# Performance work log

Hardware: AMD Instinct MI355X
Metric: run time of the kernel (lower is better)

The kernel has to match this reference:

```python
import jax, jax.numpy as jnp
import numpy as np

B, L = 512, 8192          # batch, document length
N = 128                   # output_sentence_num
S = 256                   # output_sentence_len
DELIM = 5                 # delimiter token
PAD = 0                   # pad_word
CUT_HEAD = False
VOCAB = 100


def setup_inputs() -> dict:
    key = jax.random.key(0)
    x = jax.random.randint(key, (B, L), 0, VOCAB, dtype=jnp.int32)
    return {"x": x}


def reference(x):
    b, l = x.shape
    # right-padded row: original tokens + one trailing delimiter, shape [B, L+1]
    rpad = jnp.concatenate([x, jnp.full((b, 1), DELIM, x.dtype)], axis=1)
    # segment id of rpad position j = number of delimiters in x[:j]
    cum = jnp.cumsum((x == DELIM).astype(jnp.int32), axis=1)           # [B, L]
    seg = jnp.concatenate([jnp.zeros((b, 1), jnp.int32), cum], axis=1)  # [B, L+1]
    seg = jnp.minimum(seg, N - 1)  # segments >= N-1 merged into last chunk (tail merge)
    j = jnp.arange(l + 1, dtype=jnp.int32)
    bidx = jnp.arange(b)[:, None]
    # start index of each segment (min j with seg==k); unused segments stay at L+1
    starts = jnp.full((b, N), l + 1, jnp.int32)
    starts = starts.at[bidx, seg].min(jnp.broadcast_to(j, (b, l + 1)))
    pos = j[None, :] - jnp.take_along_axis(starts, seg, axis=1)  # offset within chunk
    # chunk sizes (number of rpad positions per segment)
    sizes = jnp.zeros((b, N), jnp.int32).at[bidx, seg].add(jnp.ones((b, l + 1), jnp.int32))
    size_here = jnp.take_along_axis(sizes, seg, axis=1)
    # size-1 chunks (lone delimiter == empty sentence) are filled with pad_word
    vals = jnp.where(size_here == 1, jnp.int32(PAD), rpad)
    if CUT_HEAD:
        p = pos - 1
        valid = (pos >= 1) & (pos <= S - 1)  # chunk[1:S], then padded to S
    else:
        p = pos
        valid = pos <= S - 1                 # chunk[:S]
    # scatter into [B, N, S]; invalid positions routed out-of-bounds and dropped
    k_idx = jnp.where(valid, seg, N)
    p_idx = jnp.where(valid, p, S)
    otp = jnp.full((b, N, S), PAD, x.dtype)
    otp = otp.at[bidx, k_idx, p_idx].set(vals, mode='drop')
    # lengths / mask (tf.count_nonzero semantics; pad_word == 0)
    len_sent = jnp.sum((otp != 0).astype(jnp.int32), axis=2)   # [B, N]
    len_doc = jnp.sum((len_sent != 0).astype(jnp.int32), axis=1)  # [B]
    mask = (jnp.arange(S)[None, None, :] < len_sent[..., None]).astype(jnp.float32)
    return otp, len_doc, mask
```

## Files before the change

### kernel.cpp

```cpp
#include <hip/hip_runtime.h>

#define B_ 512
#define L_ 8192
#define N_ 128
#define S_ 256
#define DELIM_ 5
#define T_ 1024
#define NW_ (T_ / 64)

__device__ __forceinline__ int sw_idx(int p) { return p ^ ((p >> 5) & 3); }

__global__ __launch_bounds__(T_, 8) void split_kernel(const int* __restrict__ x,
                                                      float* __restrict__ otp,
                                                      float* __restrict__ len_doc,
                                                      float* __restrict__ mask) {
    const int b = blockIdx.x;
    const int t = threadIdx.x;
    const int lane = t & 63;
    const int w = t >> 6;
    const int* __restrict__ row = x + (size_t)b * L_;

    __shared__ __align__(16) int s_row[L_ + 1];
    __shared__ int s_wsum[NW_];
    __shared__ int s_dpos[N_ - 1];
    __shared__ int s_start[N_];
    __shared__ int s_cl[N_];
    __shared__ int s_doc[NW_];

    const int4 r0 = ((const int4*)row)[t];
    const int4 r1 = ((const int4*)row)[t + T_];

    const int v = (t >> 3) & 3;
    int4 w0 = r0, w1 = r1;
    if (v == 1)      { w0 = make_int4(r0.y, r0.x, r0.w, r0.z); w1 = make_int4(r1.y, r1.x, r1.w, r1.z); }
    else if (v == 2) { w0 = make_int4(r0.z, r0.w, r0.x, r0.y); w1 = make_int4(r1.z, r1.w, r1.x, r1.y); }
    else if (v == 3) { w0 = make_int4(r0.w, r0.z, r0.y, r0.x); w1 = make_int4(r1.w, r1.z, r1.y, r1.x); }
    ((int4*)s_row)[t] = w0;
    ((int4*)s_row)[t + T_] = w1;
    if (t == 0) s_row[L_] = DELIM_;

    const int c0 = (r0.x == DELIM_) + (r0.y == DELIM_) + (r0.z == DELIM_) + (r0.w == DELIM_);
    const int c1 = (r1.x == DELIM_) + (r1.y == DELIM_) + (r1.z == DELIM_) + (r1.w == DELIM_);
    const int packed = c0 | (c1 << 16);

    int sv = packed;
#pragma unroll
    for (int d = 1; d < 64; d <<= 1) {
        int n = __shfl_up(sv, d, 64);
        if (lane >= d) sv += n;
    }
    if (lane == 63) s_wsum[w] = sv;
    __syncthreads();

    int woff = 0, tot = 0;
#pragma unroll
    for (int i = 0; i < NW_; ++i) {
        const int s = s_wsum[i];
        if (i < w) woff += s;
        tot += s;
    }
    const int pre = woff + sv - packed;
    const int c0tot = tot & 0xffff;
    const int m = c0tot + (tot >> 16);
    const int off0 = pre & 0xffff;
    const int off1 = c0tot + (pre >> 16);

    if (c0 > 0 && off0 < N_ - 1) {
        int o = off0;
        const int p = 4 * t;
        if (r0.x == DELIM_) { if (o < N_ - 1) s_dpos[o] = p;     ++o; }
        if (r0.y == DELIM_) { if (o < N_ - 1) s_dpos[o] = p + 1; ++o; }
        if (r0.z == DELIM_) { if (o < N_ - 1) s_dpos[o] = p + 2; ++o; }
        if (r0.w == DELIM_) { if (o < N_ - 1) s_dpos[o] = p + 3; ++o; }
    }
    if (c1 > 0 && off1 < N_ - 1) {
        int o = off1;
        const int p = 4 * T_ + 4 * t;
        if (r1.x == DELIM_) { if (o < N_ - 1) s_dpos[o] = p;     ++o; }
        if (r1.y == DELIM_) { if (o < N_ - 1) s_dpos[o] = p + 1; ++o; }
        if (r1.z == DELIM_) { if (o < N_ - 1) s_dpos[o] = p + 2; ++o; }
        if (r1.w == DELIM_) { if (o < N_ - 1) s_dpos[o] = p + 3; ++o; }
    }
    __syncthreads();

    if (t < N_) {
        const int k = t;
        const int mc = (m < N_ - 1) ? m : (N_ - 1);
        int start = 0, cl = 0;
        if (k <= mc) {
            start = (k == 0) ? 0 : (s_dpos[k - 1] + 1);
            const int end = (k < mc) ? s_dpos[k] : L_;
            const int size = end - start + 1;
            cl = (size <= 1) ? 0 : (size < S_ ? size : S_);
        }
        s_start[k] = start;
        s_cl[k] = cl;
    }
    __syncthreads();

    float* __restrict__ otp_b = otp + (size_t)b * N_ * S_;
    float* __restrict__ msk_b = mask + (size_t)b * N_ * S_;
    int doccnt = 0;
    const int e0 = lane << 2;
#pragma unroll
    for (int i = 0; i < (N_ / NW_); ++i) {
        const int k = i * NW_ + w;
        const int start = s_start[k];
        const int cl = s_cl[k];
        float4 tf = make_float4(0.f, 0.f, 0.f, 0.f);
        float4 mk = make_float4(0.f, 0.f, 0.f, 0.f);
        int len = 0;
        if (cl > 0) {
            int t0 = 0, t1 = 0, t2 = 0, t3 = 0;
            if (e0 + 0 < cl) t0 = s_row[sw_idx(start + e0 + 0)];
            if (e0 + 1 < cl) t1 = s_row[sw_idx(start + e0 + 1)];
            if (e0 + 2 < cl) t2 = s_row[sw_idx(start + e0 + 2)];
            if (e0 + 3 < cl) t3 = s_row[sw_idx(start + e0 + 3)];
            len += __popcll(__ballot(t0 != 0));
            len += __popcll(__ballot(t1 != 0));
            len += __popcll(__ballot(t2 != 0));
            len += __popcll(__ballot(t3 != 0));
            tf = make_float4((float)t0, (float)t1, (float)t2, (float)t3);
            mk = make_float4(e0 + 0 < len ? 1.f : 0.f, e0 + 1 < len ? 1.f : 0.f,
                             e0 + 2 < len ? 1.f : 0.f, e0 + 3 < len ? 1.f : 0.f);
        }
        ((float4*)(otp_b + (size_t)k * S_))[lane] = tf;
        ((float4*)(msk_b + (size_t)k * S_))[lane] = mk;
        doccnt += (len > 0);
    }

    if (lane == 0) s_doc[w] = doccnt;
    __syncthreads();
    if (t == 0) {
        int d = 0;
#pragma unroll
        for (int i = 0; i < NW_; ++i) d += s_doc[i];
        len_doc[b] = (float)d;
    }
}

extern "C" void kernel_launch(void* const* d_in, const int* in_sizes, int n_in,
                              void* d_out, int out_size, void* d_ws, size_t ws_size,
                              hipStream_t stream) {
    const int* x = (const int*)d_in[0];
    float* out = (float*)d_out;

    float* otp = out;
    float* len_doc = out + (size_t)B_ * N_ * S_;
    float* mask = len_doc + B_;

    split_kernel<<<B_, T_, 0, stream>>>(x, otp, len_doc, mask);
}
```

Baseline: 142.6 us.

## Split into table-building kernel and wide write kernel using workspace

Result: slower. 146.2 us (+2.5%).

```diff
diff --git a/kernel.cpp b/kernel.cpp
--- a/kernel.cpp
+++ b/kernel.cpp
@@ -5,39 +5,24 @@
 #define N_ 128
 #define S_ 256
 #define DELIM_ 5
-#define T_ 1024
-#define NW_ (T_ / 64)
-
-__device__ __forceinline__ int sw_idx(int p) { return p ^ ((p >> 5) & 3); }
-
-__global__ __launch_bounds__(T_, 8) void split_kernel(const int* __restrict__ x,
-                                                      float* __restrict__ otp,
-                                                      float* __restrict__ len_doc,
-                                                      float* __restrict__ mask) {
+#define TA_ 1024
+#define NWA_ (TA_ / 64)
+#define TB_ 256
+
+__global__ __launch_bounds__(TA_) void table_kernel(const int* __restrict__ x,
+                                                    int2* __restrict__ tbl,
+                                                    float* __restrict__ len_doc) {
     const int b = blockIdx.x;
     const int t = threadIdx.x;
     const int lane = t & 63;
     const int w = t >> 6;
     const int* __restrict__ row = x + (size_t)b * L_;
 
-    __shared__ __align__(16) int s_row[L_ + 1];
-    __shared__ int s_wsum[NW_];
+    __shared__ int s_wsum[NWA_];
     __shared__ int s_dpos[N_ - 1];
-    __shared__ int s_start[N_];
-    __shared__ int s_cl[N_];
-    __shared__ int s_doc[NW_];
 
     const int4 r0 = ((const int4*)row)[t];
-    const int4 r1 = ((const int4*)row)[t + T_];
-
-    const int v = (t >> 3) & 3;
-    int4 w0 = r0, w1 = r1;
-    if (v == 1)      { w0 = make_int4(r0.y, r0.x, r0.w, r0.z); w1 = make_int4(r1.y, r1.x, r1.w, r1.z); }
-    else if (v == 2) { w0 = make_int4(r0.z, r0.w, r0.x, r0.y); w1 = make_int4(r1.z, r1.w, r1.x, r1.y); }
-    else if (v == 3) { w0 = make_int4(r0.w, r0.z, r0.y, r0.x); w1 = make_int4(r1.w, r1.z, r1.y, r1.x); }
-    ((int4*)s_row)[t] = w0;
-    ((int4*)s_row)[t + T_] = w1;
-    if (t == 0) s_row[L_] = DELIM_;
+    const int4 r1 = ((const int4*)row)[t + TA_];
 
     const int c0 = (r0.x == DELIM_) + (r0.y == DELIM_) + (r0.z == DELIM_) + (r0.w == DELIM_);
     const int c1 = (r1.x == DELIM_) + (r1.y == DELIM_) + (r1.z == DELIM_) + (r1.w == DELIM_);
@@ -54,7 +39,7 @@
 
     int woff = 0, tot = 0;
 #pragma unroll
-    for (int i = 0; i < NW_; ++i) {
+    for (int i = 0; i < NWA_; ++i) {
         const int s = s_wsum[i];
         if (i < w) woff += s;
         tot += s;
@@ -75,7 +60,7 @@
     }
     if (c1 > 0 && off1 < N_ - 1) {
         int o = off1;
-        const int p = 4 * T_ + 4 * t;
+        const int p = 4 * TA_ + 4 * t;
         if (r1.x == DELIM_) { if (o < N_ - 1) s_dpos[o] = p;     ++o; }
         if (r1.y == DELIM_) { if (o < N_ - 1) s_dpos[o] = p + 1; ++o; }
         if (r1.z == DELIM_) { if (o < N_ - 1) s_dpos[o] = p + 2; ++o; }
@@ -93,6 +78,159 @@
             const int size = end - start + 1;
             cl = (size <= 1) ? 0 : (size < S_ ? size : S_);
         }
+        tbl[b * N_ + k] = make_int2(start, cl);
+    }
+    if (t == 0) len_doc[b] = 0.0f;
+}
+
+__global__ __launch_bounds__(TB_, 8) void write_kernel(const int* __restrict__ x,
+                                                       const int2* __restrict__ tbl,
+                                                       float* __restrict__ otp,
+                                                       float* __restrict__ len_doc,
+                                                       float* __restrict__ mask) {
+    const int kb = blockIdx.x;
+    const int b  = blockIdx.y;
+    const int t = threadIdx.x;
+    const int lane = t & 63;
+    const int w = t >> 6;
+    const int* __restrict__ row = x + (size_t)b * L_;
+    float* __restrict__ otp_b = otp + (size_t)b * N_ * S_;
+    float* __restrict__ msk_b = mask + (size_t)b * N_ * S_;
+    __shared__ int s_cnt[TB_ / 64];
+
+    int cnt = 0;
+#pragma unroll
+    for (int i = 0; i < 4; ++i) {
+        const int k = kb * 16 + w * 4 + i;
+        const int2 sc = tbl[b * N_ + k];
+        const int start = sc.x, cl = sc.y;
+        int tok0 = 0, tok1 = 0, tok2 = 0, tok3 = 0;
+        int len = 0;
+        if (cl > 0) {
+#pragma unroll
+            for (int j = 0; j < 4; ++j) {
+                const int e = 64 * j + lane;
+                const int idx = start + e;
+                const int a = (idx < L_) ? idx : (L_ - 1);
+                int v = row[a];
+                v = (idx == L_) ? DELIM_ : v;
+                v = (e < cl) ? v : 0;
+                if (j == 0) tok0 = v; else if (j == 1) tok1 = v;
+                else if (j == 2) tok2 = v; else tok3 = v;
+            }
+            len += __popcll(__ballot(tok0 != 0));
+            len += __popcll(__ballot(tok1 != 0));
+            len += __popcll(__ballot(tok2 != 0));
+            len += __popcll(__ballot(tok3 != 0));
+        }
+        {
+            const int e0 = lane;
+            otp_b[(size_t)k * S_ + e0]       = (float)tok0;
+            otp_b[(size_t)k * S_ + e0 + 64]  = (float)tok1;
+            otp_b[(size_t)k * S_ + e0 + 128] = (float)tok2;
+            otp_b[(size_t)k * S_ + e0 + 192] = (float)tok3;
+            msk_b[(size_t)k * S_ + e0]       = (e0       < len) ? 1.0f : 0.0f;
+            msk_b[(size_t)k * S_ + e0 + 64]  = (e0 + 64  < len) ? 1.0f : 0.0f;
+            msk_b[(size_t)k * S_ + e0 + 128] = (e0 + 128 < len) ? 1.0f : 0.0f;
+            msk_b[(size_t)k * S_ + e0 + 192] = (e0 + 192 < len) ? 1.0f : 0.0f;
+        }
+        cnt += (len > 0);
+    }
+    if (lane == 0) s_cnt[w] = cnt;
+    __syncthreads();
+    if (t == 0) {
+        int d = 0;
+#pragma unroll
+        for (int i = 0; i < TB_ / 64; ++i) d += s_cnt[i];
+        if (d) atomicAdd(&len_doc[b], (float)d);
+    }
+}
+
+__device__ __forceinline__ int sw_idx(int p) { return p ^ ((p >> 5) & 3); }
+
+__global__ __launch_bounds__(TA_, 8) void split_kernel(const int* __restrict__ x,
+                                                       float* __restrict__ otp,
+                                                       float* __restrict__ len_doc,
+                                                       float* __restrict__ mask) {
+    const int b = blockIdx.x;
+    const int t = threadIdx.x;
+    const int lane = t & 63;
+    const int w = t >> 6;
+    const int* __restrict__ row = x + (size_t)b * L_;
+
+    __shared__ __align__(16) int s_row[L_ + 1];
+    __shared__ int s_wsum[NWA_];
+    __shared__ int s_dpos[N_ - 1];
+    __shared__ int s_start[N_];
+    __shared__ int s_cl[N_];
+    __shared__ int s_doc[NWA_];
+
+    const int4 r0 = ((const int4*)row)[t];
+    const int4 r1 = ((const int4*)row)[t + TA_];
+
+    const int v = (t >> 3) & 3;
+    int4 w0 = r0, w1 = r1;
+    if (v == 1)      { w0 = make_int4(r0.y, r0.x, r0.w, r0.z); w1 = make_int4(r1.y, r1.x, r1.w, r1.z); }
+    else if (v == 2) { w0 = make_int4(r0.z, r0.w, r0.x, r0.y); w1 = make_int4(r1.z, r1.w, r1.x, r1.y); }
+    else if (v == 3) { w0 = make_int4(r0.w, r0.z, r0.y, r0.x); w1 = make_int4(r1.w, r1.z, r1.y, r1.x); }
+    ((int4*)s_row)[t] = w0;
+    ((int4*)s_row)[t + TA_] = w1;
+    if (t == 0) s_row[L_] = DELIM_;
+
+    const int c0 = (r0.x == DELIM_) + (r0.y == DELIM_) + (r0.z == DELIM_) + (r0.w == DELIM_);
+    const int c1 = (r1.x == DELIM_) + (r1.y == DELIM_) + (r1.z == DELIM_) + (r1.w == DELIM_);
+    const int packed = c0 | (c1 << 16);
+
+    int sv = packed;
+#pragma unroll
+    for (int d = 1; d < 64; d <<= 1) {
+        int n = __shfl_up(sv, d, 64);
+        if (lane >= d) sv += n;
+    }
+    if (lane == 63) s_wsum[w] = sv;
+    __syncthreads();
+
+    int woff = 0, tot = 0;
+#pragma unroll
+    for (int i = 0; i < NWA_; ++i) {
+        const int s = s_wsum[i];
+        if (i < w) woff += s;
+        tot += s;
+    }
+    const int pre = woff + sv - packed;
+    const int c0tot = tot & 0xffff;
+    const int m = c0tot + (tot >> 16);
+    const int off0 = pre & 0xffff;
+    const int off1 = c0tot + (pre >> 16);
+
+    if (c0 > 0 && off0 < N_ - 1) {
+        int o = off0;
+        const int p = 4 * t;
+        if (r0.x == DELIM_) { if (o < N_ - 1) s_dpos[o] = p;     ++o; }
+        if (r0.y == DELIM_) { if (o < N_ - 1) s_dpos[o] = p + 1; ++o; }
+        if (r0.z == DELIM_) { if (o < N_ - 1) s_dpos[o] = p + 2; ++o; }
+        if (r0.w == DELIM_) { if (o < N_ - 1) s_dpos[o] = p + 3; ++o; }
+    }
+    if (c1 > 0 && off1 < N_ - 1) {
+        int o = off1;
+        const int p = 4 * TA_ + 4 * t;
+        if (r1.x == DELIM_) { if (o < N_ - 1) s_dpos[o] = p;     ++o; }
+        if (r1.y == DELIM_) { if (o < N_ - 1) s_dpos[o] = p + 1; ++o; }
+        if (r1.z == DELIM_) { if (o < N_ - 1) s_dpos[o] = p + 2; ++o; }
+        if (r1.w == DELIM_) { if (o < N_ - 1) s_dpos[o] = p + 3; ++o; }
+    }
+    __syncthreads();
+
+    if (t < N_) {
+        const int k = t;
+        const int mc = (m < N_ - 1) ? m : (N_ - 1);
+        int start = 0, cl = 0;
+        if (k <= mc) {
+            start = (k == 0) ? 0 : (s_dpos[k - 1] + 1);
+            const int end = (k < mc) ? s_dpos[k] : L_;
+            const int size = end - start + 1;
+            cl = (size <= 1) ? 0 : (size < S_ ? size : S_);
+        }
         s_start[k] = start;
         s_cl[k] = cl;
     }
@@ -103,19 +241,23 @@
     int doccnt = 0;
     const int e0 = lane << 2;
 #pragma unroll
-    for (int i = 0; i < (N_ / NW_); ++i) {
-        const int k = i * NW_ + w;
+    for (int i = 0; i < (N_ / NWA_); ++i) {
+        const int k = i * NWA_ + w;
         const int start = s_start[k];
         const int cl = s_cl[k];
         float4 tf = make_float4(0.f, 0.f, 0.f, 0.f);
         float4 mk = make_float4(0.f, 0.f, 0.f, 0.f);
         int len = 0;
         if (cl > 0) {
-            int t0 = 0, t1 = 0, t2 = 0, t3 = 0;
-            if (e0 + 0 < cl) t0 = s_row[sw_idx(start + e0 + 0)];
-            if (e0 + 1 < cl) t1 = s_row[sw_idx(start + e0 + 1)];
-            if (e0 + 2 < cl) t2 = s_row[sw_idx(start + e0 + 2)];
-            if (e0 + 3 < cl) t3 = s_row[sw_idx(start + e0 + 3)];
+            const int cm = cl - 1;
+            int t0 = s_row[sw_idx(start + (e0 + 0 <= cm ? e0 + 0 : cm))];
+            int t1 = s_row[sw_idx(start + (e0 + 1 <= cm ? e0 + 1 : cm))];
+            int t2 = s_row[sw_idx(start + (e0 + 2 <= cm ? e0 + 2 : cm))];
+            int t3 = s_row[sw_idx(start + (e0 + 3 <= cm ? e0 + 3 : cm))];
+            t0 = (e0 + 0 < cl) ? t0 : 0;
+            t1 = (e0 + 1 < cl) ? t1 : 0;
+            t2 = (e0 + 2 < cl) ? t2 : 0;
+            t3 = (e0 + 3 < cl) ? t3 : 0;
             len += __popcll(__ballot(t0 != 0));
             len += __popcll(__ballot(t1 != 0));
             len += __popcll(__ballot(t2 != 0));
@@ -134,7 +276,7 @@
     if (t == 0) {
         int d = 0;
 #pragma unroll
-        for (int i = 0; i < NW_; ++i) d += s_doc[i];
+        for (int i = 0; i < NWA_; ++i) d += s_doc[i];
         len_doc[b] = (float)d;
     }
 }
@@ -149,5 +291,12 @@
     float* len_doc = out + (size_t)B_ * N_ * S_;
     float* mask = len_doc + B_;
 
-    split_kernel<<<B_, T_, 0, stream>>>(x, otp, len_doc, mask);
+    const size_t tbl_bytes = (size_t)B_ * N_ * sizeof(int2);
+    if (d_ws != nullptr && ws_size >= tbl_bytes) {
+        int2* tbl = (int2*)d_ws;
+        table_kernel<<<B_, TA_, 0, stream>>>(x, tbl, len_doc);
+        write_kernel<<<dim3(8, B_), TB_, 0, stream>>>(x, tbl, otp, len_doc, mask);
+    } else {
+        split_kernel<<<B_, TA_, 0, stream>>>(x, otp, len_doc, mask);
+    }
 }
```

## Drop shared-memory row staging and gather chunk tokens directly from global

Applied to the files above, without the earlier changes.

New measurement: 141.9 us, median of 2. About the same (-0.5%).

```diff
diff --git a/kernel.cpp b/kernel.cpp
--- a/kernel.cpp
+++ b/kernel.cpp
@@ -7,8 +7,6 @@
 #define DELIM_ 5
 #define T_ 1024
 #define NW_ (T_ / 64)
-
-__device__ __forceinline__ int sw_idx(int p) { return p ^ ((p >> 5) & 3); }
 
 __global__ __launch_bounds__(T_, 8) void split_kernel(const int* __restrict__ x,
                                                       float* __restrict__ otp,
@@ -20,24 +18,12 @@
     const int w = t >> 6;
     const int* __restrict__ row = x + (size_t)b * L_;
 
-    __shared__ __align__(16) int s_row[L_ + 1];
     __shared__ int s_wsum[NW_];
     __shared__ int s_dpos[N_ - 1];
-    __shared__ int s_start[N_];
-    __shared__ int s_cl[N_];
     __shared__ int s_doc[NW_];
 
     const int4 r0 = ((const int4*)row)[t];
     const int4 r1 = ((const int4*)row)[t + T_];
-
-    const int v = (t >> 3) & 3;
-    int4 w0 = r0, w1 = r1;
-    if (v == 1)      { w0 = make_int4(r0.y, r0.x, r0.w, r0.z); w1 = make_int4(r1.y, r1.x, r1.w, r1.z); }
-    else if (v == 2) { w0 = make_int4(r0.z, r0.w, r0.x, r0.y); w1 = make_int4(r1.z, r1.w, r1.x, r1.y); }
-    else if (v == 3) { w0 = make_int4(r0.w, r0.z, r0.y, r0.x); w1 = make_int4(r1.w, r1.z, r1.y, r1.x); }
-    ((int4*)s_row)[t] = w0;
-    ((int4*)s_row)[t + T_] = w1;
-    if (t == 0) s_row[L_] = DELIM_;
 
     const int c0 = (r0.x == DELIM_) + (r0.y == DELIM_) + (r0.z == DELIM_) + (r0.w == DELIM_);
     const int c1 = (r1.x == DELIM_) + (r1.y == DELIM_) + (r1.z == DELIM_) + (r1.w == DELIM_);
@@ -83,49 +69,60 @@
     }
     __syncthreads();
 
-    if (t < N_) {
-        const int k = t;
-        const int mc = (m < N_ - 1) ? m : (N_ - 1);
-        int start = 0, cl = 0;
+    const int mc = (m < N_ - 1) ? m : (N_ - 1);
+    float* __restrict__ otp_b = otp + (size_t)b * N_ * S_;
+    float* __restrict__ msk_b = mask + (size_t)b * N_ * S_;
+    int doccnt = 0;
+#pragma unroll
+    for (int i = 0; i < (N_ / NW_); ++i) {
+        const int k = i * NW_ + w;
+        int cl = 0, start = 0;
         if (k <= mc) {
             start = (k == 0) ? 0 : (s_dpos[k - 1] + 1);
             const int end = (k < mc) ? s_dpos[k] : L_;
             const int size = end - start + 1;
             cl = (size <= 1) ? 0 : (size < S_ ? size : S_);
         }
-        s_start[k] = start;
-        s_cl[k] = cl;
-    }
-    __syncthreads();
-
-    float* __restrict__ otp_b = otp + (size_t)b * N_ * S_;
-    float* __restrict__ msk_b = mask + (size_t)b * N_ * S_;
-    int doccnt = 0;
-    const int e0 = lane << 2;
-#pragma unroll
-    for (int i = 0; i < (N_ / NW_); ++i) {
-        const int k = i * NW_ + w;
-        const int start = s_start[k];
-        const int cl = s_cl[k];
-        float4 tf = make_float4(0.f, 0.f, 0.f, 0.f);
-        float4 mk = make_float4(0.f, 0.f, 0.f, 0.f);
+        int t0 = 0, t1 = 0, t2 = 0, t3 = 0;
         int len = 0;
         if (cl > 0) {
-            int t0 = 0, t1 = 0, t2 = 0, t3 = 0;
-            if (e0 + 0 < cl) t0 = s_row[sw_idx(start + e0 + 0)];
-            if (e0 + 1 < cl) t1 = s_row[sw_idx(start + e0 + 1)];
-            if (e0 + 2 < cl) t2 = s_row[sw_idx(start + e0 + 2)];
-            if (e0 + 3 < cl) t3 = s_row[sw_idx(start + e0 + 3)];
+            {
+                const int idx = start + lane;
+                int v0 = row[idx < L_ ? idx : L_ - 1];
+                v0 = (idx == L_) ? DELIM_ : v0;
+                t0 = (lane < cl) ? v0 : 0;
+            }
+            {
+                const int idx = start + 64 + lane;
+                int v1 = row[idx < L_ ? idx : L_ - 1];
+                v1 = (idx == L_) ? DELIM_ : v1;
+                t1 = (64 + lane < cl) ? v1 : 0;
+            }
+            {
+                const int idx = start + 128 + lane;
+                int v2 = row[idx < L_ ? idx : L_ - 1];
+                v2 = (idx == L_) ? DELIM_ : v2;
+                t2 = (128 + lane < cl) ? v2 : 0;
+            }
+            {
+                const int idx = start + 192 + lane;
+                int v3 = row[idx < L_ ? idx : L_ - 1];
+                v3 = (idx == L_) ? DELIM_ : v3;
+                t3 = (192 + lane < cl) ? v3 : 0;
+            }
             len += __popcll(__ballot(t0 != 0));
             len += __popcll(__ballot(t1 != 0));
             len += __popcll(__ballot(t2 != 0));
             len += __popcll(__ballot(t3 != 0));
-            tf = make_float4((float)t0, (float)t1, (float)t2, (float)t3);
-            mk = make_float4(e0 + 0 < len ? 1.f : 0.f, e0 + 1 < len ? 1.f : 0.f,
-                             e0 + 2 < len ? 1.f : 0.f, e0 + 3 < len ? 1.f : 0.f);
         }
-        ((float4*)(otp_b + (size_t)k * S_))[lane] = tf;
-        ((float4*)(msk_b + (size_t)k * S_))[lane] = mk;
+        otp_b[(size_t)k * S_ + lane]       = (float)t0;
+        otp_b[(size_t)k * S_ + lane + 64]  = (float)t1;
+        otp_b[(size_t)k * S_ + lane + 128] = (float)t2;
+        otp_b[(size_t)k * S_ + lane + 192] = (float)t3;
+        msk_b[(size_t)k * S_ + lane]       = (lane       < len) ? 1.0f : 0.0f;
+        msk_b[(size_t)k * S_ + lane + 64]  = (lane + 64  < len) ? 1.0f : 0.0f;
+        msk_b[(size_t)k * S_ + lane + 128] = (lane + 128 < len) ? 1.0f : 0.0f;
+        msk_b[(size_t)k * S_ + lane + 192] = (lane + 192 < len) ? 1.0f : 0.0f;
         doccnt += (len > 0);
     }
 
```
